# Performance work log

Hardware: AMD Instinct MI355X
Metric: run time of the kernel (lower is better)

## Reference

```python
import jax, jax.numpy as jnp
import numpy as np

NUM_HEADS = 12
TEMPORAL_RES = 8


def _ln(x, g, b, eps=1e-5):
    mu = jnp.mean(x, axis=-1, keepdims=True)
    var = jnp.mean((x - mu) ** 2, axis=-1, keepdims=True)
    return (x - mu) * jax.lax.rsqrt(var + eps) * g + b


def setup_inputs() -> dict:
    key = jax.random.key(0)
    ks = jax.random.split(key, 8)
    s = 0.02
    d = 768
    inp = {
        'box_tensors': jax.random.uniform(ks[0], (16, 16, 10, 4), dtype=jnp.float32),
        'box_categories': jax.random.normal(ks[1], (16, 10, d), dtype=jnp.float32) * s,
        'w1': jax.random.normal(ks[2], (4, d // 2), dtype=jnp.float32) * s,
        'w2': jax.random.normal(ks[3], (d // 2, d), dtype=jnp.float32) * s,
        'ln1_g': jnp.ones((d,), jnp.float32),
        'ln1_b': jnp.zeros((d,), jnp.float32),
        'wqkv': jax.random.normal(ks[4], (d, 3 * d), dtype=jnp.float32) * s,
        'wo': jax.random.normal(ks[5], (d, d), dtype=jnp.float32) * s,
        'bo': jnp.zeros((d,), jnp.float32),
        'ln2_g': jnp.ones((d,), jnp.float32),
        'ln2_b': jnp.zeros((d,), jnp.float32),
        'wfc1': jax.random.normal(ks[6], (d, 4 * d), dtype=jnp.float32) * s,
        'bfc1': jnp.zeros((4 * d,), jnp.float32),
        'wfc2': jax.random.normal(ks[7], (4 * d, d), dtype=jnp.float32) * s,
        'bfc2': jnp.zeros((d,), jnp.float32),
        'H': 14,
        'W': 14,
    }
    return inp


def _forward(box_tensors, box_categories, w1, w2, ln1_g, ln1_b, wqkv, wo, bo,
             ln2_g, ln2_b, wfc1, bfc1, wfc2, bfc2, H, W):
    B, T, O, _ = box_tensors.shape
    d = box_categories.shape[-1]
    # coord -> feature MLP (no biases), then pos-emb add
    h = jax.nn.relu(box_tensors @ w1)
    x = jax.nn.relu(h @ w2)                      # [B,T,O,d]
    x = x + box_categories[None]                 # broadcast over batch
    L = T * O
    x = x.reshape(B, L, d)
    # --- self-attention block (pre-LN ViT style) ---
    hn = _ln(x, ln1_g, ln1_b)
    qkv = (hn @ wqkv).reshape(B, L, 3, NUM_HEADS, d // NUM_HEADS)
    q, k, v = qkv[:, :, 0], qkv[:, :, 1], qkv[:, :, 2]   # [B,L,h,dh]
    scale = 1.0 / jnp.sqrt(jnp.asarray(d // NUM_HEADS, x.dtype))
    att = jnp.einsum('bqhd,bkhd->bhqk', q, k) * scale
    att = jax.nn.softmax(att, axis=-1)
    o = jnp.einsum('bhqk,bkhd->bqhd', att, v).reshape(B, L, d)
    x = x + (o @ wo + bo)
    hn = _ln(x, ln2_g, ln2_b)
    x = x + (jax.nn.gelu(hn @ wfc1 + bfc1, approximate=False) @ wfc2 + bfc2)
    feats = x.reshape(B, T, O, d)
    # --- box2spatial layout scatter: sum each object's feature into grid cells inside its box ---
    x1 = jnp.minimum(box_tensors[..., 0], box_tensors[..., 2])
    x2 = jnp.maximum(box_tensors[..., 0], box_tensors[..., 2])
    y1 = jnp.minimum(box_tensors[..., 1], box_tensors[..., 3])
    y2 = jnp.maximum(box_tensors[..., 1], box_tensors[..., 3])
    cy = (jnp.arange(H, dtype=x.dtype) + 0.5) / H    # [H]
    cx = (jnp.arange(W, dtype=x.dtype) + 0.5) / W    # [W]
    in_y = (cy[None, None, None, :] >= y1[..., None]) & (cy[None, None, None, :] <= y2[..., None])  # [B,T,O,H]
    in_x = (cx[None, None, None, :] >= x1[..., None]) & (cx[None, None, None, :] <= x2[..., None])  # [B,T,O,W]
    mask = (in_y[..., :, None] & in_x[..., None, :]).astype(x.dtype)  # [B,T,O,H,W]
    grid = jnp.einsum('btohw,btod->bthwd', mask, feats)               # [B,T,H,W,d]
    # temporal avg pooling to TEMPORAL_RES frames
    Tr = T // TEMPORAL_RES
    if Tr > 1:
        grid = grid.reshape(B, T // Tr, Tr, H, W, d).mean(axis=2)
    return grid.reshape(B, -1, d)                 # [B, T'*H*W, d]


def reference(box_tensors, box_categories, w1, w2, ln1_g, ln1_b, wqkv, wo, bo,
              ln2_g, ln2_b, wfc1, bfc1, wfc2, bfc2, H, W):
    return _forward(box_tensors, box_categories, w1, w2, ln1_g, ln1_b, wqkv, wo, bo,
                    ln2_g, ln2_b, wfc1, bfc1, wfc2, bfc2, H, W)
```

## Files before the change

kernel.cpp:

```cpp
#include <hip/hip_runtime.h>
#include <hip/hip_bf16.h>
#include <math.h>


#define BATCH 16
#define TT    16
#define OO    10
#define LL    160
#define BL    2560
#define DD    768
#define NH    12
#define DH    64
#define GH    14
#define GW    14
#define TGRP  8

typedef unsigned short ushort_t;
typedef __attribute__((ext_vector_type(8))) __bf16 bf16x8;
typedef __attribute__((ext_vector_type(4))) float f32x4;

__device__ __forceinline__ ushort_t f2bf(float f) {
    unsigned int u = __float_as_uint(f);
    u += 0x7fffu + ((u >> 16) & 1u);
    return (ushort_t)(u >> 16);
}

__global__ __launch_bounds__(256)
void transpose_w(const float* __restrict__ W, ushort_t* __restrict__ Wt, int K, int N)
{
    __shared__ float s[32][33];
    const int n0 = blockIdx.x * 32, k0 = blockIdx.y * 32;
    const int tx = threadIdx.x & 31, ty = threadIdx.x >> 5;
#pragma unroll
    for (int r = 0; r < 4; ++r)
        s[ty + r * 8][tx] = W[(size_t)(k0 + ty + r * 8) * N + n0 + tx];
    __syncthreads();
#pragma unroll
    for (int r = 0; r < 4; ++r)
        Wt[(size_t)(n0 + ty + r * 8) * K + k0 + tx] = f2bf(s[tx][ty + r * 8]);
}

__global__ __launch_bounds__(256)
void box_h(const float* __restrict__ box, const float* __restrict__ w1,
           ushort_t* __restrict__ h)
{
    const int idx = blockIdx.x * 256 + threadIdx.x;
    const int r = idx / 384, j = idx - r * 384;
    const float* bx = box + (size_t)r * 4;
    float v = bx[0] * w1[j] + bx[1] * w1[384 + j] +
              bx[2] * w1[768 + j] + bx[3] * w1[1152 + j];
    h[idx] = f2bf(fmaxf(v, 0.f));
}

__global__ __launch_bounds__(256)
void ln_kernel(const float* __restrict__ in, const float* __restrict__ g,
               const float* __restrict__ bvec, ushort_t* __restrict__ out)
{
    const int r = blockIdx.x;
    const int tid = threadIdx.x;
    const float* row = in + (size_t)r * DD;
    float v0 = row[tid], v1 = row[tid + 256], v2 = row[tid + 512];
    float s  = v0 + v1 + v2;
    float s2 = v0 * v0 + v1 * v1 + v2 * v2;
#pragma unroll
    for (int off = 32; off > 0; off >>= 1) {
        s  += __shfl_down(s, off);
        s2 += __shfl_down(s2, off);
    }
    __shared__ float red[8];
    int wave = tid >> 6, lane = tid & 63;
    if (lane == 0) { red[wave] = s; red[wave + 4] = s2; }
    __syncthreads();
    s  = red[0] + red[1] + red[2] + red[3];
    s2 = red[4] + red[5] + red[6] + red[7];
    float mu  = s * (1.f / DD);
    float var = s2 * (1.f / DD) - mu * mu;
    float inv = rsqrtf(var + 1e-5f);
    ushort_t* op = out + (size_t)r * DD;
    op[tid]       = f2bf((v0 - mu) * inv * g[tid]       + bvec[tid]);
    op[tid + 256] = f2bf((v1 - mu) * inv * g[tid + 256] + bvec[tid + 256]);
    op[tid + 512] = f2bf((v2 - mu) * inv * g[tid + 512] + bvec[tid + 512]);
}

#define LOADF(aa, bb, kk)                                                        \
    _Pragma("unroll")                                                            \
    for (int i = 0; i < 4; ++i) {                                                \
        aa[i] = *reinterpret_cast<const bf16x8*>(ap + (size_t)(i * 16) * lda + (kk)); \
        bb[i] = *reinterpret_cast<const bf16x8*>(bp + (size_t)(i * 16) * ldb + (kk)); \
    }
#define MFMA16(aa, bb)                                                           \
    _Pragma("unroll")                                                            \
    for (int i = 0; i < 4; ++i)                                                  \
        _Pragma("unroll")                                                        \
        for (int j = 0; j < 4; ++j)                                              \
            acc[i][j] = __builtin_amdgcn_mfma_f32_16x16x32_bf16(aa[i], bb[j], acc[i][j], 0, 0, 0);

template <int MODE, int SPLIT>
__global__ __launch_bounds__(64)
void gemm_rf(const ushort_t* __restrict__ A, int lda,
             const ushort_t* __restrict__ Bt, int ldb,
             const float* __restrict__ bias, const float* __restrict__ cat,
             float* __restrict__ Cf, ushort_t* __restrict__ Cb,
             int ldc, int K)
{
    const int lane = threadIdx.x;
    const int l16 = lane & 15, quad = lane >> 4;
    const int row0 = blockIdx.y * 64, col0 = blockIdx.x * 64;
    const int Kper = K / SPLIT;
    const int k0 = blockIdx.z * Kper;

    const ushort_t* ap = A  + (size_t)(row0 + l16) * lda + k0 + quad * 8;
    const ushort_t* bp = Bt + (size_t)(col0 + l16) * ldb + k0 + quad * 8;

    f32x4 acc[4][4];
#pragma unroll
    for (int i = 0; i < 4; ++i)
#pragma unroll
        for (int j = 0; j < 4; ++j) {
            acc[i][j][0] = 0.f; acc[i][j][1] = 0.f;
            acc[i][j][2] = 0.f; acc[i][j][3] = 0.f;
        }

    bf16x8 a0[4], b0[4], a1[4], b1[4];
    LOADF(a0, b0, 0)
    int kt = 0;
    for (; kt + 64 < Kper; kt += 64) {
        LOADF(a1, b1, kt + 32)
        MFMA16(a0, b0)
        LOADF(a0, b0, kt + 64)
        MFMA16(a1, b1)
    }
    LOADF(a1, b1, kt + 32)
    MFMA16(a0, b0)
    MFMA16(a1, b1)

    const int q4 = quad * 4;
#pragma unroll
    for (int i = 0; i < 4; ++i)
#pragma unroll
        for (int j = 0; j < 4; ++j) {
            const int gcol = col0 + j * 16 + l16;
            const float bj = (MODE == 1 || MODE == 2)
                               ? ((SPLIT == 1 || blockIdx.z == 0) ? bias[gcol] : 0.f)
                               : 0.f;
#pragma unroll
            for (int r = 0; r < 4; ++r) {
                const int grow = row0 + i * 16 + q4 + r;
                const size_t idx = (size_t)grow * ldc + gcol;
                const float v = acc[i][j][r];
                if (MODE == 1) {
                    if (SPLIT > 1) atomicAdd(&Cf[idx], v + bj);
                    else           Cf[idx] += v + bj;
                } else if (MODE == 2) {
                    const float u = v + bj;
                    Cb[idx] = f2bf(0.5f * u * (1.f + erff(u * 0.70710678118654752f)));
                } else if (MODE == 3) {
                    Cb[idx] = f2bf(v);
                } else {
                    Cf[idx] = fmaxf(v, 0.f) + cat[(size_t)(grow % LL) * DD + gcol];
                }
            }
        }
}

#define KS_STRIDE 72
#define VT_STRIDE 168
__global__ __launch_bounds__(320)
void attention_mfma(ushort_t* __restrict__ qkv)
{
    __shared__ ushort_t Ks[160 * KS_STRIDE];
    __shared__ ushort_t Vt[64 * VT_STRIDE];
    __shared__ ushort_t Pb[5][32 * VT_STRIDE];

    const int b  = blockIdx.x / NH;
    const int hh = blockIdx.x % NH;
    ushort_t* basew = qkv + (size_t)b * LL * (3 * DD) + hh * DH;
    const ushort_t* base = basew;
    const int tid  = threadIdx.x;
    const int wave = tid >> 6, lane = tid & 63;
    const int l16 = lane & 15, quad = lane >> 4;

#pragma unroll
    for (int it = 0; it < 4; ++it) {
        int idx = tid + it * 320;
        int l = idx >> 3, c8 = (idx & 7) * 8;
        uint4 kv = *(const uint4*)(base + (size_t)l * (3 * DD) + DD + c8);
        *(uint4*)&Ks[l * KS_STRIDE + c8] = kv;
        uint4 vv = *(const uint4*)(base + (size_t)l * (3 * DD) + 2 * DD + c8);
        ushort_t e[8];
        *(uint4*)e = vv;
#pragma unroll
        for (int i = 0; i < 8; ++i)
            Vt[(c8 + i) * VT_STRIDE + l] = e[i];
    }

    const int q0 = wave * 32;
    bf16x8 qf[2][2];
#pragma unroll
    for (int t = 0; t < 2; ++t)
#pragma unroll
        for (int k = 0; k < 2; ++k)
            qf[t][k] = *reinterpret_cast<const bf16x8*>(
                base + (size_t)(q0 + t * 16 + l16) * (3 * DD) + k * 32 + quad * 8);

    __syncthreads();

    f32x4 S0[10], S1[10];
#pragma unroll
    for (int nt = 0; nt < 10; ++nt) {
        f32x4 z = {0.f, 0.f, 0.f, 0.f};
        const ushort_t* kb = &Ks[(nt * 16 + l16) * KS_STRIDE + quad * 8];
        bf16x8 kf0 = *reinterpret_cast<const bf16x8*>(kb);
        bf16x8 kf1 = *reinterpret_cast<const bf16x8*>(kb + 32);
        f32x4 a0 = __builtin_amdgcn_mfma_f32_16x16x32_bf16(qf[0][0], kf0, z, 0, 0, 0);
        S0[nt]   = __builtin_amdgcn_mfma_f32_16x16x32_bf16(qf[0][1], kf1, a0, 0, 0, 0);
        f32x4 a1 = __builtin_amdgcn_mfma_f32_16x16x32_bf16(qf[1][0], kf0, z, 0, 0, 0);
        S1[nt]   = __builtin_amdgcn_mfma_f32_16x16x32_bf16(qf[1][1], kf1, a1, 0, 0, 0);
    }

#pragma unroll
    for (int t = 0; t < 2; ++t) {
        f32x4* S = t ? S1 : S0;
        float mrow[4] = {-1e30f, -1e30f, -1e30f, -1e30f};
#pragma unroll
        for (int nt = 0; nt < 10; ++nt)
#pragma unroll
            for (int r = 0; r < 4; ++r) {
                S[nt][r] *= 0.125f;
                mrow[r] = fmaxf(mrow[r], S[nt][r]);
            }
#pragma unroll
        for (int r = 0; r < 4; ++r) {
            mrow[r] = fmaxf(mrow[r], __shfl_xor(mrow[r], 1));
            mrow[r] = fmaxf(mrow[r], __shfl_xor(mrow[r], 2));
            mrow[r] = fmaxf(mrow[r], __shfl_xor(mrow[r], 4));
            mrow[r] = fmaxf(mrow[r], __shfl_xor(mrow[r], 8));
        }
        float lsum[4] = {0.f, 0.f, 0.f, 0.f};
#pragma unroll
        for (int nt = 0; nt < 10; ++nt)
#pragma unroll
            for (int r = 0; r < 4; ++r) {
                float e = __expf(S[nt][r] - mrow[r]);
                S[nt][r] = e;
                lsum[r] += e;
            }
#pragma unroll
        for (int r = 0; r < 4; ++r) {
            lsum[r] += __shfl_xor(lsum[r], 1);
            lsum[r] += __shfl_xor(lsum[r], 2);
            lsum[r] += __shfl_xor(lsum[r], 4);
            lsum[r] += __shfl_xor(lsum[r], 8);
            lsum[r] = 1.f / lsum[r];
        }
#pragma unroll
        for (int nt = 0; nt < 10; ++nt)
#pragma unroll
            for (int r = 0; r < 4; ++r)
                Pb[wave][(t * 16 + quad * 4 + r) * VT_STRIDE + nt * 16 + l16] =
                    f2bf(S[nt][r] * lsum[r]);
    }
    asm volatile("s_waitcnt lgkmcnt(0)" ::: "memory");

#pragma unroll
    for (int dt = 0; dt < 4; ++dt) {
        f32x4 o0 = {0.f, 0.f, 0.f, 0.f}, o1 = {0.f, 0.f, 0.f, 0.f};
#pragma unroll
        for (int ks = 0; ks < 5; ++ks) {
            bf16x8 vf = *reinterpret_cast<const bf16x8*>(
                &Vt[(dt * 16 + l16) * VT_STRIDE + ks * 32 + quad * 8]);
            bf16x8 p0 = *reinterpret_cast<const bf16x8*>(
                &Pb[wave][(l16) * VT_STRIDE + ks * 32 + quad * 8]);
            bf16x8 p1 = *reinterpret_cast<const bf16x8*>(
                &Pb[wave][(16 + l16) * VT_STRIDE + ks * 32 + quad * 8]);
            o0 = __builtin_amdgcn_mfma_f32_16x16x32_bf16(vf, p0, o0, 0, 0, 0);
            o1 = __builtin_amdgcn_mfma_f32_16x16x32_bf16(vf, p1, o1, 0, 0, 0);
        }
#pragma unroll
        for (int t = 0; t < 2; ++t) {
            f32x4 o = t ? o1 : o0;
            ushort_t pk[4];
#pragma unroll
            for (int r = 0; r < 4; ++r) pk[r] = f2bf(o[r]);
            ushort_t* dst = basew + (size_t)(q0 + t * 16 + l16) * (3 * DD) +
                            dt * 16 + quad * 4;
            *(uint2*)dst = *(const uint2*)pk;
        }
    }
}

__global__ __launch_bounds__(256)
void mask_grid(const float* __restrict__ box, const float* __restrict__ feats,
               float* __restrict__ out)
{
    const int hw = blockIdx.x;
    const int g  = blockIdx.y;
    const int b  = blockIdx.z;
    const int hh = hw / GW, w = hw % GW;
    const float cy = (hh + 0.5f) / (float)GH;
    const float cx = (w  + 0.5f) / (float)GW;
    const int tid = threadIdx.x;

    __shared__ float flg[20];
    if (tid < 20) {
        int t = g * 2 + tid / OO, o = tid % OO;
        const float* bx = box + (size_t)((b * TT + t) * OO + o) * 4;
        float x1 = fminf(bx[0], bx[2]), x2 = fmaxf(bx[0], bx[2]);
        float y1 = fminf(bx[1], bx[3]), y2 = fmaxf(bx[1], bx[3]);
        flg[tid] = (cy >= y1 && cy <= y2 && cx >= x1 && cx <= x2) ? 1.f : 0.f;
    }
    __syncthreads();

    float a0 = 0.f, a1 = 0.f, a2 = 0.f;
#pragma unroll
    for (int p = 0; p < 20; ++p) {
        if (flg[p] != 0.f) {
            int r = (b * TT + g * 2 + p / OO) * OO + (p % OO);
            const float* f = feats + (size_t)r * DD;
            a0 += f[tid]; a1 += f[tid + 256]; a2 += f[tid + 512];
        }
    }
    float* op = out + ((size_t)b * (TGRP * GH * GW) + g * (GH * GW) + hw) * DD;
    op[tid]       = a0 * 0.5f;
    op[tid + 256] = a1 * 0.5f;
    op[tid + 512] = a2 * 0.5f;
}

extern "C" void kernel_launch(void* const* d_in, const int* in_sizes, int n_in,
                              void* d_out, int out_size, void* d_ws, size_t ws_size,
                              hipStream_t stream)
{
    const float* box  = (const float*)d_in[0];
    const float* cat  = (const float*)d_in[1];
    const float* w1   = (const float*)d_in[2];
    const float* w2   = (const float*)d_in[3];
    const float* ln1g = (const float*)d_in[4];
    const float* ln1b = (const float*)d_in[5];
    const float* wqkv = (const float*)d_in[6];
    const float* wo   = (const float*)d_in[7];
    const float* bo   = (const float*)d_in[8];
    const float* ln2g = (const float*)d_in[9];
    const float* ln2b = (const float*)d_in[10];
    const float* wfc1 = (const float*)d_in[11];
    const float* bfc1 = (const float*)d_in[12];
    const float* wfc2 = (const float*)d_in[13];
    const float* bfc2 = (const float*)d_in[14];
    float* out = (float*)d_out;

    char* wsb = (char*)d_ws;
    float*    x     = (float*)   (wsb + 0);
    ushort_t* qkvb  = (ushort_t*)(wsb + 7864320);
    ushort_t* fc1b  = qkvb;
    ushort_t* hnb   = (ushort_t*)(wsb + 23592960);
    ushort_t* wqkvT = (ushort_t*)(wsb + 27525120);
    ushort_t* woT   = (ushort_t*)(wsb + 31064064);
    ushort_t* wfc1T = (ushort_t*)(wsb + 32243712);
    ushort_t* wfc2T = (ushort_t*)(wsb + 36962304);
    ushort_t* w2T   = (ushort_t*)(wsb + 41680896);
    ushort_t* h     = (ushort_t*)(wsb + 42270720);

    transpose_w<<<dim3(2304 / 32, 768 / 32), 256, 0, stream>>>(wqkv, wqkvT, 768, 2304);
    transpose_w<<<dim3(768 / 32, 768 / 32), 256, 0, stream>>>(wo, woT, 768, 768);
    transpose_w<<<dim3(3072 / 32, 768 / 32), 256, 0, stream>>>(wfc1, wfc1T, 768, 3072);
    transpose_w<<<dim3(768 / 32, 3072 / 32), 256, 0, stream>>>(wfc2, wfc2T, 3072, 768);
    transpose_w<<<dim3(768 / 32, 384 / 32), 256, 0, stream>>>(w2, w2T, 384, 768);

    box_h<<<BL * 384 / 256, 256, 0, stream>>>(box, w1, h);
    gemm_rf<4, 1><<<dim3(12, 40, 1), 64, 0, stream>>>(h, 384, w2T, 384, nullptr, cat,
                                                      x, nullptr, DD, 384);
    ln_kernel<<<BL, 256, 0, stream>>>(x, ln1g, ln1b, hnb);
    gemm_rf<3, 1><<<dim3(36, 40, 1), 64, 0, stream>>>(hnb, DD, wqkvT, DD, nullptr, nullptr,
                                                      nullptr, qkvb, 3 * DD, DD);
    attention_mfma<<<BATCH * NH, 320, 0, stream>>>(qkvb);
    gemm_rf<1, 2><<<dim3(12, 40, 2), 64, 0, stream>>>(qkvb, 3 * DD, woT, DD, bo, nullptr,
                                                      x, nullptr, DD, DD);
    ln_kernel<<<BL, 256, 0, stream>>>(x, ln2g, ln2b, hnb);
    gemm_rf<2, 1><<<dim3(48, 40, 1), 64, 0, stream>>>(hnb, DD, wfc1T, DD, bfc1, nullptr,
                                                      nullptr, fc1b, 4 * DD, DD);
    gemm_rf<1, 4><<<dim3(12, 40, 4), 64, 0, stream>>>(fc1b, 4 * DD, wfc2T, 4 * DD, bfc2, nullptr,
                                                      x, nullptr, DD, 4 * DD);
    mask_grid<<<dim3(GH * GW, TGRP, BATCH), 256, 0, stream>>>(box, x, out);
}
```

Before: 372.2 us.

## Shrink GEMM tiles with XCD swizzle, replace atomic split-K, restructure mask_grid

GEMMs move to a templated kernel with smaller per-wave tiles (32x32 or 32x64) and a block-index swizzle that spreads consecutive workgroups across XCDs. Wo no longer uses split-K. FC2 writes two partial buffers that a separate vectorized kernel sums with the bias and residual, replacing float atomics. mask_grid now stages the 20 feature rows in shared memory once per block and loops over 49 grid cells, so far fewer blocks reread the same features. The trade-offs are more blocks with less reuse per wave, an extra reduction pass, and about 60KB of LDS per mask_grid block, which lowers occupancy.

```diff
diff --git a/kernel.cpp b/kernel.cpp
--- a/kernel.cpp
+++ b/kernel.cpp
@@ -23,6 +23,10 @@
     unsigned int u = __float_as_uint(f);
     u += 0x7fffu + ((u >> 16) & 1u);
     return (ushort_t)(u >> 16);
+}
+
+__device__ __forceinline__ int swz_xcd(int bid, int nwg) {
+    return (bid & 7) * (nwg >> 3) + (bid >> 3);
 }
 
 __global__ __launch_bounds__(256)
@@ -82,85 +86,109 @@
     op[tid + 512] = f2bf((v2 - mu) * inv * g[tid + 512] + bvec[tid + 512]);
 }
 
-#define LOADF(aa, bb, kk)                                                        \
-    _Pragma("unroll")                                                            \
-    for (int i = 0; i < 4; ++i) {                                                \
-        aa[i] = *reinterpret_cast<const bf16x8*>(ap + (size_t)(i * 16) * lda + (kk)); \
-        bb[i] = *reinterpret_cast<const bf16x8*>(bp + (size_t)(i * 16) * ldb + (kk)); \
-    }
-#define MFMA16(aa, bb)                                                           \
-    _Pragma("unroll")                                                            \
-    for (int i = 0; i < 4; ++i)                                                  \
-        _Pragma("unroll")                                                        \
-        for (int j = 0; j < 4; ++j)                                              \
-            acc[i][j] = __builtin_amdgcn_mfma_f32_16x16x32_bf16(aa[i], bb[j], acc[i][j], 0, 0, 0);
-
-template <int MODE, int SPLIT>
+template <int MI, int NJ, int MODE, int SPLIT>
 __global__ __launch_bounds__(64)
-void gemm_rf(const ushort_t* __restrict__ A, int lda,
-             const ushort_t* __restrict__ Bt, int ldb,
-             const float* __restrict__ bias, const float* __restrict__ cat,
-             float* __restrict__ Cf, ushort_t* __restrict__ Cb,
-             int ldc, int K)
+void gemm_rf2(const ushort_t* __restrict__ A, int lda,
+              const ushort_t* __restrict__ Bt, int ldb,
+              const float* __restrict__ bias, const float* __restrict__ cat,
+              float* __restrict__ Cf, ushort_t* __restrict__ Cb,
+              int ldc, int K)
 {
     const int lane = threadIdx.x;
     const int l16 = lane & 15, quad = lane >> 4;
-    const int row0 = blockIdx.y * 64, col0 = blockIdx.x * 64;
+
+    const int nwg = gridDim.x * gridDim.y * gridDim.z;
+    const int bid = blockIdx.x + gridDim.x * (blockIdx.y + gridDim.y * blockIdx.z);
+    const int w   = swz_xcd(bid, nwg);
+    const int bx  = w % gridDim.x;
+    const int byz = w / gridDim.x;
+    const int by  = byz % gridDim.y;
+    const int bz  = byz / gridDim.y;
+
+    const int row0 = by * (MI * 16), col0 = bx * (NJ * 16);
     const int Kper = K / SPLIT;
-    const int k0 = blockIdx.z * Kper;
+    const int k0   = bz * Kper;
 
     const ushort_t* ap = A  + (size_t)(row0 + l16) * lda + k0 + quad * 8;
     const ushort_t* bp = Bt + (size_t)(col0 + l16) * ldb + k0 + quad * 8;
 
-    f32x4 acc[4][4];
-#pragma unroll
-    for (int i = 0; i < 4; ++i)
-#pragma unroll
-        for (int j = 0; j < 4; ++j) {
+    f32x4 acc[MI][NJ];
+#pragma unroll
+    for (int i = 0; i < MI; ++i)
+#pragma unroll
+        for (int j = 0; j < NJ; ++j) {
             acc[i][j][0] = 0.f; acc[i][j][1] = 0.f;
             acc[i][j][2] = 0.f; acc[i][j][3] = 0.f;
         }
 
-    bf16x8 a0[4], b0[4], a1[4], b1[4];
-    LOADF(a0, b0, 0)
+#define LOADF2(aa, bb, kk)                                                       \
+    _Pragma("unroll")                                                            \
+    for (int i = 0; i < MI; ++i)                                                 \
+        aa[i] = *reinterpret_cast<const bf16x8*>(ap + (size_t)(i * 16) * lda + (kk)); \
+    _Pragma("unroll")                                                            \
+    for (int j = 0; j < NJ; ++j)                                                 \
+        bb[j] = *reinterpret_cast<const bf16x8*>(bp + (size_t)(j * 16) * ldb + (kk));
+#define MFMA2(aa, bb)                                                            \
+    _Pragma("unroll")                                                            \
+    for (int i = 0; i < MI; ++i)                                                 \
+        _Pragma("unroll")                                                        \
+        for (int j = 0; j < NJ; ++j)                                             \
+            acc[i][j] = __builtin_amdgcn_mfma_f32_16x16x32_bf16(aa[i], bb[j], acc[i][j], 0, 0, 0);
+
+    bf16x8 a0[MI], b0[NJ], a1[MI], b1[NJ];
+    LOADF2(a0, b0, 0)
     int kt = 0;
     for (; kt + 64 < Kper; kt += 64) {
-        LOADF(a1, b1, kt + 32)
-        MFMA16(a0, b0)
-        LOADF(a0, b0, kt + 64)
-        MFMA16(a1, b1)
-    }
-    LOADF(a1, b1, kt + 32)
-    MFMA16(a0, b0)
-    MFMA16(a1, b1)
+        LOADF2(a1, b1, kt + 32)
+        MFMA2(a0, b0)
+        LOADF2(a0, b0, kt + 64)
+        MFMA2(a1, b1)
+    }
+    LOADF2(a1, b1, kt + 32)
+    MFMA2(a0, b0)
+    MFMA2(a1, b1)
+#undef LOADF2
+#undef MFMA2
 
     const int q4 = quad * 4;
 #pragma unroll
-    for (int i = 0; i < 4; ++i)
-#pragma unroll
-        for (int j = 0; j < 4; ++j) {
+    for (int i = 0; i < MI; ++i)
+#pragma unroll
+        for (int j = 0; j < NJ; ++j) {
             const int gcol = col0 + j * 16 + l16;
-            const float bj = (MODE == 1 || MODE == 2)
-                               ? ((SPLIT == 1 || blockIdx.z == 0) ? bias[gcol] : 0.f)
-                               : 0.f;
+            const float bj = (MODE == 1 || MODE == 2) ? bias[gcol] : 0.f;
 #pragma unroll
             for (int r = 0; r < 4; ++r) {
                 const int grow = row0 + i * 16 + q4 + r;
                 const size_t idx = (size_t)grow * ldc + gcol;
                 const float v = acc[i][j][r];
                 if (MODE == 1) {
-                    if (SPLIT > 1) atomicAdd(&Cf[idx], v + bj);
-                    else           Cf[idx] += v + bj;
+                    Cf[idx] += v + bj;
                 } else if (MODE == 2) {
                     const float u = v + bj;
                     Cb[idx] = f2bf(0.5f * u * (1.f + erff(u * 0.70710678118654752f)));
                 } else if (MODE == 3) {
                     Cb[idx] = f2bf(v);
+                } else if (MODE == 4) {
+                    Cf[idx] = fmaxf(v, 0.f) + cat[(size_t)(grow % LL) * DD + gcol];
                 } else {
-                    Cf[idx] = fmaxf(v, 0.f) + cat[(size_t)(grow % LL) * DD + gcol];
+                    Cf[(size_t)bz * (BL * DD) + idx] = v;
                 }
             }
         }
+}
+
+__global__ __launch_bounds__(256)
+void reduce_fc2(const float* __restrict__ P, const float* __restrict__ bias,
+                float* __restrict__ x)
+{
+    const int i4 = (blockIdx.x * 256 + threadIdx.x) * 4;
+    f32x4 a  = *reinterpret_cast<const f32x4*>(&x[i4]);
+    f32x4 p0 = *reinterpret_cast<const f32x4*>(&P[i4]);
+    f32x4 p1 = *reinterpret_cast<const f32x4*>(&P[BL * DD + i4]);
+    f32x4 b  = *reinterpret_cast<const f32x4*>(&bias[i4 % DD]);
+    a = a + p0 + p1 + b;
+    *reinterpret_cast<f32x4*>(&x[i4]) = a;
 }
 
 #define KS_STRIDE 72
@@ -293,37 +321,47 @@
 void mask_grid(const float* __restrict__ box, const float* __restrict__ feats,
                float* __restrict__ out)
 {
-    const int hw = blockIdx.x;
-    const int g  = blockIdx.y;
-    const int b  = blockIdx.z;
-    const int hh = hw / GW, w = hw % GW;
-    const float cy = (hh + 0.5f) / (float)GH;
-    const float cx = (w  + 0.5f) / (float)GW;
+    const int chunk = blockIdx.x;
+    const int g = blockIdx.y;
+    const int b = blockIdx.z;
     const int tid = threadIdx.x;
 
-    __shared__ float flg[20];
+    __shared__ float fs[20][DD];
+    __shared__ float x1s[20], x2s[20], y1s[20], y2s[20];
+
+#pragma unroll 4
+    for (int p = 0; p < 20; ++p) {
+        int r = (b * TT + g * 2 + p / OO) * OO + (p % OO);
+        const float* f = feats + (size_t)r * DD;
+        fs[p][tid]       = f[tid];
+        fs[p][tid + 256] = f[tid + 256];
+        fs[p][tid + 512] = f[tid + 512];
+    }
     if (tid < 20) {
         int t = g * 2 + tid / OO, o = tid % OO;
         const float* bx = box + (size_t)((b * TT + t) * OO + o) * 4;
-        float x1 = fminf(bx[0], bx[2]), x2 = fmaxf(bx[0], bx[2]);
-        float y1 = fminf(bx[1], bx[3]), y2 = fmaxf(bx[1], bx[3]);
-        flg[tid] = (cy >= y1 && cy <= y2 && cx >= x1 && cx <= x2) ? 1.f : 0.f;
+        x1s[tid] = fminf(bx[0], bx[2]); x2s[tid] = fmaxf(bx[0], bx[2]);
+        y1s[tid] = fminf(bx[1], bx[3]); y2s[tid] = fmaxf(bx[1], bx[3]);
     }
     __syncthreads();
 
-    float a0 = 0.f, a1 = 0.f, a2 = 0.f;
-#pragma unroll
-    for (int p = 0; p < 20; ++p) {
-        if (flg[p] != 0.f) {
-            int r = (b * TT + g * 2 + p / OO) * OO + (p % OO);
-            const float* f = feats + (size_t)r * DD;
-            a0 += f[tid]; a1 += f[tid + 256]; a2 += f[tid + 512];
-        }
-    }
-    float* op = out + ((size_t)b * (TGRP * GH * GW) + g * (GH * GW) + hw) * DD;
-    op[tid]       = a0 * 0.5f;
-    op[tid + 256] = a1 * 0.5f;
-    op[tid + 512] = a2 * 0.5f;
+    for (int q = 0; q < 49; ++q) {
+        const int hw = chunk * 49 + q;
+        const int hh = hw / GW, w = hw % GW;
+        const float cy = (hh + 0.5f) / (float)GH;
+        const float cx = (w  + 0.5f) / (float)GW;
+        float a0 = 0.f, a1 = 0.f, a2 = 0.f;
+#pragma unroll
+        for (int p = 0; p < 20; ++p) {
+            if (cy >= y1s[p] && cy <= y2s[p] && cx >= x1s[p] && cx <= x2s[p]) {
+                a0 += fs[p][tid]; a1 += fs[p][tid + 256]; a2 += fs[p][tid + 512];
+            }
+        }
+        float* op = out + ((size_t)b * (TGRP * GH * GW) + g * (GH * GW) + hw) * DD;
+        op[tid]       = a0 * 0.5f;
+        op[tid + 256] = a1 * 0.5f;
+        op[tid + 512] = a2 * 0.5f;
+    }
 }
 
 extern "C" void kernel_launch(void* const* d_in, const int* in_sizes, int n_in,
@@ -351,13 +389,14 @@
     float*    x     = (float*)   (wsb + 0);
     ushort_t* qkvb  = (ushort_t*)(wsb + 7864320);
     ushort_t* fc1b  = qkvb;
-    ushort_t* hnb   = (ushort_t*)(wsb + 23592960);
-    ushort_t* wqkvT = (ushort_t*)(wsb + 27525120);
-    ushort_t* woT   = (ushort_t*)(wsb + 31064064);
-    ushort_t* wfc1T = (ushort_t*)(wsb + 32243712);
-    ushort_t* wfc2T = (ushort_t*)(wsb + 36962304);
+    ushort_t* wfc2T = (ushort_t*)(wsb + 23592960);
+    ushort_t* hnb   = (ushort_t*)(wsb + 28311552);
+    ushort_t* wqkvT = (ushort_t*)(wsb + 32243712);
+    ushort_t* woT   = (ushort_t*)(wsb + 35782656);
+    ushort_t* wfc1T = (ushort_t*)(wsb + 36962304);
     ushort_t* w2T   = (ushort_t*)(wsb + 41680896);
     ushort_t* h     = (ushort_t*)(wsb + 42270720);
+    float*    fc2P  = (float*)   (wsb + 28311552);
 
     transpose_w<<<dim3(2304 / 32, 768 / 32), 256, 0, stream>>>(wqkv, wqkvT, 768, 2304);
     transpose_w<<<dim3(768 / 32, 768 / 32), 256, 0, stream>>>(wo, woT, 768, 768);
@@ -366,18 +405,19 @@
     transpose_w<<<dim3(768 / 32, 384 / 32), 256, 0, stream>>>(w2, w2T, 384, 768);
 
     box_h<<<BL * 384 / 256, 256, 0, stream>>>(box, w1, h);
-    gemm_rf<4, 1><<<dim3(12, 40, 1), 64, 0, stream>>>(h, 384, w2T, 384, nullptr, cat,
-                                                      x, nullptr, DD, 384);
+    gemm_rf2<2, 2, 4, 1><<<dim3(24, 80, 1), 64, 0, stream>>>(
+        h, 384, w2T, 384, nullptr, cat, x, nullptr, DD, 384);
     ln_kernel<<<BL, 256, 0, stream>>>(x, ln1g, ln1b, hnb);
-    gemm_rf<3, 1><<<dim3(36, 40, 1), 64, 0, stream>>>(hnb, DD, wqkvT, DD, nullptr, nullptr,
-                                                      nullptr, qkvb, 3 * DD, DD);
+    gemm_rf2<2, 4, 3, 1><<<dim3(36, 80, 1), 64, 0, stream>>>(
+        hnb, DD, wqkvT, DD, nullptr, nullptr, nullptr, qkvb, 3 * DD, DD);
     attention_mfma<<<BATCH * NH, 320, 0, stream>>>(qkvb);
-    gemm_rf<1, 2><<<dim3(12, 40, 2), 64, 0, stream>>>(qkvb, 3 * DD, woT, DD, bo, nullptr,
-                                                      x, nullptr, DD, DD);
+    gemm_rf2<2, 2, 1, 1><<<dim3(24, 80, 1), 64, 0, stream>>>(
+        qkvb, 3 * DD, woT, DD, bo, nullptr, x, nullptr, DD, DD);
     ln_kernel<<<BL, 256, 0, stream>>>(x, ln2g, ln2b, hnb);
-    gemm_rf<2, 1><<<dim3(48, 40, 1), 64, 0, stream>>>(hnb, DD, wfc1T, DD, bfc1, nullptr,
-                                                      nullptr, fc1b, 4 * DD, DD);
-    gemm_rf<1, 4><<<dim3(12, 40, 4), 64, 0, stream>>>(fc1b, 4 * DD, wfc2T, 4 * DD, bfc2, nullptr,
-                                                      x, nullptr, DD, 4 * DD);
-    mask_grid<<<dim3(GH * GW, TGRP, BATCH), 256, 0, stream>>>(box, x, out);
-}
+    gemm_rf2<2, 4, 2, 1><<<dim3(48, 80, 1), 64, 0, stream>>>(
+        hnb, DD, wfc1T, DD, bfc1, nullptr, nullptr, fc1b, 4 * DD, DD);
+    gemm_rf2<2, 2, 5, 2><<<dim3(24, 80, 2), 64, 0, stream>>>(
+        fc1b, 4 * DD, wfc2T, 4 * DD, nullptr, nullptr, fc2P, nullptr, DD, 4 * DD);
+    reduce_fc2<<<BL * DD / 4 / 256, 256, 0, stream>>>(fc2P, bfc2, x);
+    mask_grid<<<dim3(4, TGRP, BATCH), 256, 0, stream>>>(box, x, out);
+}
```

Result: slower. 458.8 us (+23.3%).
